# Kernel optimization log

Measured on AMD Instinct MI355X. Metric: run time of the kernel, lower is better.

Reference implementation:

```python
import jax, jax.numpy as jnp
import numpy as np

EPS = 1e-9
N_HEAD = 16


def clamp_c(c):
    return jnp.clip(c, 1e-4, 1.0)


def _heads(x, H):
    B, T, C = x.shape
    return x.reshape(B, T, H, C // H)


def mobius_add(x, y, c_clamped, H):
    # per-head Mobius addition; c_clamped: (H,)
    B, T, C = x.shape
    cr = c_clamped.reshape(1, 1, H, 1)
    xr, yr = _heads(x, H), _heads(y, H)
    xn = jnp.sum(xr * xr, axis=-1, keepdims=True)
    yn = jnp.sum(yr * yr, axis=-1, keepdims=True)
    ip = jnp.sum(xr * yr, axis=-1, keepdims=True)
    num = (1 + 2 * cr * ip + cr * yn) * xr + (1 - cr * xn) * yr
    den = 1 + 2 * cr * ip + cr ** 2 * xn * yn
    return (num / (den + EPS)).reshape(B, T, C)


def expmap(x, v, c, H):
    # exponential map of tangent vector v at point x (per-head curvature)
    B, T, C = x.shape
    cc = clamp_c(c)
    cr = cc.reshape(1, 1, H, 1)
    xr, vr = _heads(x, H), _heads(v, H)
    sf = 2.0 / (1 + cr * jnp.sum(xr * xr, axis=-1, keepdims=True) + EPS)  # scaling factor
    vns = jnp.sum(vr * vr, axis=-1, keepdims=True)
    vn = jnp.sqrt(vns + EPS)
    tanh_arg = jnp.abs(cr * sf * vns / 2)
    coeff = (1.0 / (jnp.sqrt(jnp.abs(cr) + EPS) + EPS)) * jnp.tanh(jnp.sqrt(tanh_arg + EPS))
    second = (coeff * vr / (vn + EPS)).reshape(B, T, C)
    return mobius_add(x, second, cc, H)


def layernorm(x, g):
    m = jnp.mean(x, axis=-1, keepdims=True)
    v = jnp.mean((x - m) ** 2, axis=-1, keepdims=True)
    return (x - m) * jax.lax.rsqrt(v + 1e-5) * g


def attention(x, w_qkv, w_proj, H):
    B, T, C = x.shape
    hs = C // H
    q, k, v = jnp.split(x @ w_qkv.T, 3, axis=-1)
    q = q.reshape(B, T, H, hs).transpose(0, 2, 1, 3)
    k = k.reshape(B, T, H, hs).transpose(0, 2, 1, 3)
    v = v.reshape(B, T, H, hs).transpose(0, 2, 1, 3)
    att = jnp.einsum('bhqd,bhkd->bhqk', q, k) * (float(hs) ** -0.5)
    mask = jnp.tril(jnp.ones((T, T), dtype=bool))
    att = jnp.where(mask, att, -jnp.inf)
    att = jax.nn.softmax(att, axis=-1)
    y = jnp.einsum('bhqk,bhkd->bhqd', att, v)
    y = y.transpose(0, 2, 1, 3).reshape(B, T, C)
    return y @ w_proj.T


def setup_inputs() -> dict:
    key = jax.random.key(0)
    ks = jax.random.split(key, 9)
    B, T, C = 2, 2048, 1024
    s = 0.02
    return {
        'x': jax.random.normal(ks[0], (B, T, C), jnp.float32) * s,
        'ln1_g': jnp.ones((C,), jnp.float32),
        'w_qkv': jax.random.normal(ks[1], (3 * C, C), jnp.float32) * s,
        'w_attn_proj': jax.random.normal(ks[2], (C, C), jnp.float32) * s,
        'c_attn': jax.random.uniform(ks[3], (N_HEAD,), jnp.float32, 0.1, 0.9),
        'ln2_g': jnp.ones((C,), jnp.float32),
        'w_fc': jax.random.normal(ks[4], (4 * C, C), jnp.float32) * s,
        'w_mlp_proj': jax.random.normal(ks[5], (C, 4 * C), jnp.float32) * s,
        'c_mlp': jax.random.uniform(ks[6], (N_HEAD,), jnp.float32, 0.1, 0.9),
    }


def reference(x, ln1_g, w_qkv, w_attn_proj, c_attn, ln2_g, w_fc, w_mlp_proj, c_mlp):
    H = N_HEAD
    a = attention(layernorm(x, ln1_g), w_qkv, w_attn_proj, H)
    x = expmap(x, a, c_attn, H)  # hyperbolic residual (attn)
    h = jax.nn.gelu(layernorm(x, ln2_g) @ w_fc.T, approximate=False) @ w_mlp_proj.T
    x = expmap(x, h, c_mlp, H)   # hyperbolic residual (mlp)
    return x
```

## Files before the change

### kernel.cpp

```cpp
#include <hip/hip_runtime.h>
#include <hip/hip_bf16.h>

typedef __attribute__((ext_vector_type(8))) short bf16x8;
typedef __attribute__((ext_vector_type(4))) float f32x4;

typedef const __attribute__((address_space(1))) void gv_t;
typedef __attribute__((address_space(3))) void lv_t;
#define GLL16(g, l) __builtin_amdgcn_global_load_lds((gv_t*)(g), (lv_t*)(l), 16, 0, 0)

__device__ __forceinline__ short f2bf(float f) {
    __hip_bfloat16 h = __float2bfloat16(f);
    return *reinterpret_cast<short*>(&h);
}

__device__ __forceinline__ float wred(float v) {
    #pragma unroll
    for (int m = 1; m < 64; m <<= 1) v += __shfl_xor(v, m);
    return v;
}

__global__ __launch_bounds__(256) void cvt_kernel(const float* __restrict__ in,
                                                  short* __restrict__ out, int n4) {
    int i = blockIdx.x * 256 + threadIdx.x;
    if (i < n4) {
        float4 v = ((const float4*)in)[i];
        short4 o;
        o.x = f2bf(v.x); o.y = f2bf(v.y); o.z = f2bf(v.z); o.w = f2bf(v.w);
        ((short4*)out)[i] = o;
    }
}

__global__ __launch_bounds__(256) void ln_kernel(const float* __restrict__ x,
                                                 const float* __restrict__ g,
                                                 short* __restrict__ y) {
    const int row = blockIdx.x, tid = threadIdx.x;
    const float4 v = ((const float4*)(x + (size_t)row * 1024))[tid];
    float s = v.x + v.y + v.z + v.w;
    float s2 = v.x * v.x + v.y * v.y + v.z * v.z + v.w * v.w;
    #pragma unroll
    for (int m = 1; m < 64; m <<= 1) { s += __shfl_xor(s, m); s2 += __shfl_xor(s2, m); }
    __shared__ float rs[4], rs2[4];
    if ((tid & 63) == 0) { rs[tid >> 6] = s; rs2[tid >> 6] = s2; }
    __syncthreads();
    s = rs[0] + rs[1] + rs[2] + rs[3];
    s2 = rs2[0] + rs2[1] + rs2[2] + rs2[3];
    const float mean = s * (1.0f / 1024.0f);
    const float var = s2 * (1.0f / 1024.0f) - mean * mean;
    const float r = rsqrtf(var + 1e-5f);
    const float4 gg = ((const float4*)g)[tid];
    short4 o;
    o.x = f2bf((v.x - mean) * r * gg.x);
    o.y = f2bf((v.y - mean) * r * gg.y);
    o.z = f2bf((v.z - mean) * r * gg.z);
    o.w = f2bf((v.w - mean) * r * gg.w);
    ((short4*)y)[(size_t)row * 256 + tid] = o;
}

template <int EPI>
__global__ __launch_bounds__(256, 2) void gemm_bt(const short* __restrict__ A,
                                                  const short* __restrict__ Bw,
                                                  int M, int N, int K,
                                                  void* __restrict__ o0,
                                                  void* __restrict__ o1,
                                                  void* __restrict__ o2) {
    __shared__ __align__(16) short As[2][128 * 64];
    __shared__ __align__(16) short Bs[2][128 * 64];
    const int tid = threadIdx.x;
    const int wid = tid >> 6, lane = tid & 63;
    const int wm = wid >> 1, wn = wid & 1;
    const int col = lane & 15, grp = lane >> 4;
    const int r8 = lane >> 3, s8 = lane & 7;
    const int m0 = blockIdx.x * 128, n0 = blockIdx.y * 128;
    f32x4 acc[4][4] = {};
    const short* ga = A + (size_t)m0 * K;
    const short* gb = Bw + (size_t)n0 * K;

#define GSTAGE(b_, t_) do {                                                     \
        const int k0_ = (t_) * 64;                                              \
        _Pragma("unroll")                                                       \
        for (int c = 0; c < 4; ++c) {                                           \
            const int row = c * 32 + wid * 8 + r8;                              \
            const int slot = s8 ^ (row & 7);                                    \
            GLL16(ga + (size_t)row * K + k0_ + slot * 8,                        \
                  (char*)&As[b_][0] + c * 4096 + wid * 1024);                   \
            GLL16(gb + (size_t)row * K + k0_ + slot * 8,                        \
                  (char*)&Bs[b_][0] + c * 4096 + wid * 1024);                   \
        }                                                                       \
    } while (0)

    const int NT = K >> 6;
    GSTAGE(0, 0);
    __syncthreads();
    int buf = 0;
    for (int t = 0; t < NT; ++t) {
        if (t + 1 < NT) GSTAGE(buf ^ 1, t + 1);
        const char* At = (const char*)&As[buf][0];
        const char* Bt = (const char*)&Bs[buf][0];
        #pragma unroll
        for (int s = 0; s < 2; ++s) {
            bf16x8 af[4], bfr[4];
            #pragma unroll
            for (int i = 0; i < 4; ++i) {
                const int rowA = wm * 64 + i * 16 + col;
                const int rowB = wn * 64 + i * 16 + col;
                af[i]  = *(const bf16x8*)(At + rowA * 128 + (((s * 4 + grp) ^ (rowA & 7)) << 4));
                bfr[i] = *(const bf16x8*)(Bt + rowB * 128 + (((s * 4 + grp) ^ (rowB & 7)) << 4));
            }
            #pragma unroll
            for (int mi = 0; mi < 4; ++mi)
                #pragma unroll
                for (int ni = 0; ni < 4; ++ni)
                    acc[mi][ni] = __builtin_amdgcn_mfma_f32_16x16x32_bf16(af[mi], bfr[ni], acc[mi][ni], 0, 0, 0);
        }
        __syncthreads();
        buf ^= 1;
    }
#undef GSTAGE
    #pragma unroll
    for (int mi = 0; mi < 4; ++mi) {
        #pragma unroll
        for (int ni = 0; ni < 4; ++ni) {
            #pragma unroll
            for (int i = 0; i < 4; ++i) {
                const int m = m0 + wm * 64 + mi * 16 + grp * 4 + i;
                const int n = n0 + wn * 64 + ni * 16 + col;
                const float v = acc[mi][ni][i];
                if (EPI == 0) {
                    const int b = m >> 11, t = m & 2047;
                    const int which = n >> 10, nn = n & 1023;
                    const int h = nn >> 6, d = nn & 63;
                    const size_t bh = (size_t)(b * 16 + h);
                    if (which == 0)
                        ((short*)o0)[(bh * 2048 + t) * 64 + d] = f2bf(v * 0.125f);
                    else if (which == 1)
                        ((short*)o1)[(bh * 2048 + t) * 64 + d] = f2bf(v);
                    else
                        ((short*)o2)[(bh * 64 + d) * 2048 + t] = f2bf(v);
                } else if (EPI == 1) {
                    ((float*)o0)[(size_t)m * N + n] = v;
                } else {
                    const float gl = 0.5f * v * (1.0f + erff(v * 0.70710678118654752f));
                    ((short*)o0)[(size_t)m * N + n] = f2bf(gl);
                }
            }
        }
    }
}

__global__ __launch_bounds__(256, 3) void attn_kernel(const short* __restrict__ Q,
                                                      const short* __restrict__ Kg,
                                                      const short* __restrict__ VT,
                                                      short* __restrict__ Y) {
    __shared__ __align__(16) short Ks[2][4096];
    __shared__ __align__(16) short Vs[2][4096];
    __shared__ __align__(16) short Plds[4][16 * 72];
    const int j = 15 - blockIdx.x;
    const int bh = blockIdx.y;
    const int tid = threadIdx.x, wid = tid >> 6, lane = tid & 63;
    const int ql = lane & 15, g = lane >> 4;
    const int r8 = lane >> 3, s8 = lane & 7;
    const int q0w = j * 128 + wid * 32;
    const int lt = 2 * j + 1;
    const short* Qb = Q + (size_t)bh * 2048 * 64;
    const short* Kb = Kg + (size_t)bh * 2048 * 64;
    const short* Vb = VT + (size_t)bh * 64 * 2048;
    short* Pw = &Plds[wid][0];

    bf16x8 qf[2][2];
    #pragma unroll
    for (int qs = 0; qs < 2; ++qs) {
        qf[qs][0] = *(const bf16x8*)&Qb[(size_t)(q0w + 16 * qs + ql) * 64 + 8 * g];
        qf[qs][1] = *(const bf16x8*)&Qb[(size_t)(q0w + 16 * qs + ql) * 64 + 32 + 8 * g];
    }
    f32x4 o[2][4] = {};
    float m[2] = {-1e30f, -1e30f}, lsum[2] = {0.f, 0.f};

#define STAGE(b_, kt_) do {                                                      \
        const int kbase_ = (kt_) * 64;                                           \
        _Pragma("unroll")                                                        \
        for (int c = 0; c < 2; ++c) {                                            \
            const int row = c * 32 + wid * 8 + r8;                               \
            const int slot = s8 ^ (row & 7);                                     \
            GLL16(Kb + (size_t)(kbase_ + row) * 64 + slot * 8,                   \
                  (char*)&Ks[b_][0] + c * 4096 + wid * 1024);                    \
            GLL16(Vb + (size_t)row * 2048 + kbase_ + slot * 8,                   \
                  (char*)&Vs[b_][0] + c * 4096 + wid * 1024);                    \
        }                                                                        \
    } while (0)

    STAGE(0, 0);
    __syncthreads();
    int buf = 0;
    for (int kt = 0; kt <= lt; ++kt) {
        if (kt < lt) STAGE(buf ^ 1, kt + 1);
        const int kbase = kt * 64;
        const short* Kt = &Ks[buf][0];
        const short* Vt = &Vs[buf][0];
        bf16x8 kf[4][2];
        #pragma unroll
        for (int kb = 0; kb < 4; ++kb) {
            const int row = 16 * kb + ql;
            const int x = row & 7;
            kf[kb][0] = *(const bf16x8*)((const char*)Kt + row * 128 + ((g ^ x) << 4));
            kf[kb][1] = *(const bf16x8*)((const char*)Kt + row * 128 + (((4 + g) ^ x) << 4));
        }
        #pragma unroll
        for (int qs = 0; qs < 2; ++qs) {
            const int q0s = q0w + 16 * qs;
            if (kbase > q0s + 15) continue;
            f32x4 s[4];
            #pragma unroll
            for (int kb = 0; kb < 4; ++kb) {
                f32x4 z = {0.f, 0.f, 0.f, 0.f};
                z = __builtin_amdgcn_mfma_f32_16x16x32_bf16(kf[kb][0], qf[qs][0], z, 0, 0, 0);
                z = __builtin_amdgcn_mfma_f32_16x16x32_bf16(kf[kb][1], qf[qs][1], z, 0, 0, 0);
                s[kb] = z;
            }
            if (kbase + 63 > q0s) {
                #pragma unroll
                for (int kb = 0; kb < 4; ++kb)
                    #pragma unroll
                    for (int r = 0; r < 4; ++r)
                        if (kbase + 16 * kb + 4 * g + r > q0s + ql) s[kb][r] = -1e30f;
            }
            float t0 = fmaxf(fmaxf(s[0][0], s[0][1]), fmaxf(s[0][2], s[0][3]));
            float t1 = fmaxf(fmaxf(s[1][0], s[1][1]), fmaxf(s[1][2], s[1][3]));
            float t2 = fmaxf(fmaxf(s[2][0], s[2][1]), fmaxf(s[2][2], s[2][3]));
            float t3 = fmaxf(fmaxf(s[3][0], s[3][1]), fmaxf(s[3][2], s[3][3]));
            float tmax = fmaxf(fmaxf(t0, t1), fmaxf(t2, t3));
            tmax = fmaxf(tmax, __shfl_xor(tmax, 16));
            tmax = fmaxf(tmax, __shfl_xor(tmax, 32));
            const float mnew = fmaxf(m[qs], tmax);
            const float sc = __expf(m[qs] - mnew);
            m[qs] = mnew;
            float rsum = 0.0f;
            #pragma unroll
            for (int kb = 0; kb < 4; ++kb) {
                const float e0 = __expf(s[kb][0] - mnew);
                const float e1 = __expf(s[kb][1] - mnew);
                const float e2 = __expf(s[kb][2] - mnew);
                const float e3 = __expf(s[kb][3] - mnew);
                rsum += (e0 + e1) + (e2 + e3);
                short4 pk;
                pk.x = f2bf(e0); pk.y = f2bf(e1); pk.z = f2bf(e2); pk.w = f2bf(e3);
                *(short4*)&Pw[ql * 72 + 16 * kb + 4 * g] = pk;
            }
            rsum += __shfl_xor(rsum, 16);
            rsum += __shfl_xor(rsum, 32);
            lsum[qs] = lsum[qs] * sc + rsum;
            #pragma unroll
            for (int nf = 0; nf < 4; ++nf)
                #pragma unroll
                for (int r = 0; r < 4; ++r) o[qs][nf][r] *= sc;
            const bf16x8 pb0 = *(const bf16x8*)&Pw[ql * 72 + 8 * g];
            const bf16x8 pb1 = *(const bf16x8*)&Pw[ql * 72 + 32 + 8 * g];
            #pragma unroll
            for (int nf = 0; nf < 4; ++nf) {
                const int row = 16 * nf + ql;
                const int x = row & 7;
                bf16x8 v0 = *(const bf16x8*)((const char*)Vt + row * 128 + ((g ^ x) << 4));
                bf16x8 v1 = *(const bf16x8*)((const char*)Vt + row * 128 + (((4 + g) ^ x) << 4));
                o[qs][nf] = __builtin_amdgcn_mfma_f32_16x16x32_bf16(v0, pb0, o[qs][nf], 0, 0, 0);
                o[qs][nf] = __builtin_amdgcn_mfma_f32_16x16x32_bf16(v1, pb1, o[qs][nf], 0, 0, 0);
            }
        }
        __syncthreads();
        buf ^= 1;
    }
#undef STAGE
    const int b = bh >> 4, h = bh & 15;
    #pragma unroll
    for (int qs = 0; qs < 2; ++qs) {
        const float inv = 1.0f / lsum[qs];
        const size_t rowoff = ((size_t)b * 2048 + q0w + 16 * qs + ql) * 1024 + h * 64;
        #pragma unroll
        for (int nf = 0; nf < 4; ++nf) {
            short4 w;
            w.x = f2bf(o[qs][nf][0] * inv);
            w.y = f2bf(o[qs][nf][1] * inv);
            w.z = f2bf(o[qs][nf][2] * inv);
            w.w = f2bf(o[qs][nf][3] * inv);
            *(short4*)&Y[rowoff + 16 * nf + 4 * g] = w;
        }
    }
}

__global__ __launch_bounds__(256) void expmap_kernel(const float* __restrict__ x,
                                                     const float* __restrict__ v,
                                                     const float* __restrict__ carr,
                                                     float* __restrict__ out) {
    const int blk = blockIdx.x;
    const int row = blk >> 2;
    const int head = (blk & 3) * 4 + (threadIdx.x >> 6);
    const int lane = threadIdx.x & 63;
    const size_t idx = (size_t)row * 1024 + head * 64 + lane;
    float c = carr[head];
    c = fminf(fmaxf(c, 1e-4f), 1.0f);
    const float xe = x[idx], ve = v[idx];
    const float xn = wred(xe * xe);
    const float vns = wred(ve * ve);
    const float vn = sqrtf(vns + 1e-9f);
    const float sf = 2.0f / (1.0f + c * xn + 1e-9f);
    const float targ = fabsf(0.5f * c * sf * vns);
    const float coeff = (1.0f / (sqrtf(c + 1e-9f) + 1e-9f)) * tanhf(sqrtf(targ + 1e-9f));
    const float ye = coeff * ve / (vn + 1e-9f);
    const float yn = wred(ye * ye);
    const float ip = wred(xe * ye);
    const float num = (1.0f + 2.0f * c * ip + c * yn) * xe + (1.0f - c * xn) * ye;
    const float den = 1.0f + 2.0f * c * ip + c * c * xn * yn;
    out[idx] = num / (den + 1e-9f);
}

extern "C" void kernel_launch(void* const* d_in, const int* in_sizes, int n_in,
                              void* d_out, int out_size, void* d_ws, size_t ws_size,
                              hipStream_t stream) {
    (void)in_sizes; (void)n_in; (void)out_size; (void)ws_size;
    const float* x      = (const float*)d_in[0];
    const float* ln1_g  = (const float*)d_in[1];
    const float* w_qkv  = (const float*)d_in[2];
    const float* w_proj = (const float*)d_in[3];
    const float* c_attn = (const float*)d_in[4];
    const float* ln2_g  = (const float*)d_in[5];
    const float* w_fc   = (const float*)d_in[6];
    const float* w_mlp  = (const float*)d_in[7];
    const float* c_mlp  = (const float*)d_in[8];
    float* out = (float*)d_out;
    char* ws = (char*)d_ws;
    const size_t MB = 1024 * 1024;

    short* wqkv_bf  = (short*)(ws + 0 * MB);
    short* wproj_bf = (short*)(ws + 6 * MB);
    short* wfc_bf   = (short*)(ws + 8 * MB);
    short* wmlp_bf  = (short*)(ws + 16 * MB);
    short* y_bf     = (short*)(ws + 24 * MB);
    short* q_bf     = (short*)(ws + 32 * MB);
    short* k_bf     = (short*)(ws + 40 * MB);
    short* vT_bf    = (short*)(ws + 48 * MB);
    short* att_bf   = (short*)(ws + 56 * MB);
    float* a_f32    = (float*)(ws + 64 * MB);
    float* x1       = (float*)(ws + 80 * MB);
    short* g_bf     = (short*)(ws + 32 * MB);
    float* h_f32    = (float*)(ws + 64 * MB);

    cvt_kernel<<<3072, 256, 0, stream>>>(w_qkv, wqkv_bf, 3072 * 1024 / 4);
    cvt_kernel<<<1024, 256, 0, stream>>>(w_proj, wproj_bf, 1024 * 1024 / 4);
    cvt_kernel<<<4096, 256, 0, stream>>>(w_fc, wfc_bf, 4096 * 1024 / 4);
    cvt_kernel<<<4096, 256, 0, stream>>>(w_mlp, wmlp_bf, 1024 * 4096 / 4);

    ln_kernel<<<4096, 256, 0, stream>>>(x, ln1_g, y_bf);
    gemm_bt<0><<<dim3(32, 24), 256, 0, stream>>>(y_bf, wqkv_bf, 4096, 3072, 1024,
                                                 q_bf, k_bf, vT_bf);
    attn_kernel<<<dim3(16, 32), 256, 0, stream>>>(q_bf, k_bf, vT_bf, att_bf);
    gemm_bt<1><<<dim3(32, 8), 256, 0, stream>>>(att_bf, wproj_bf, 4096, 1024, 1024,
                                                a_f32, nullptr, nullptr);
    expmap_kernel<<<16384, 256, 0, stream>>>(x, a_f32, c_attn, x1);
    ln_kernel<<<4096, 256, 0, stream>>>(x1, ln2_g, y_bf);
    gemm_bt<2><<<dim3(32, 32), 256, 0, stream>>>(y_bf, wfc_bf, 4096, 4096, 1024,
                                                 g_bf, nullptr, nullptr);
    gemm_bt<1><<<dim3(32, 8), 256, 0, stream>>>(g_bf, wmlp_bf, 4096, 1024, 4096,
                                                h_f32, nullptr, nullptr);
    expmap_kernel<<<16384, 256, 0, stream>>>(x1, h_f32, c_mlp, out);
}
```

Baseline: 311.0 us.

## Restructure GEMM main loop into prefetch-two pipeline with explicit waitcnt barriers

The bf16 GEMM loop now preloads two K-tiles before it starts. In each iteration it reads the whole current LDS tile into registers, waits on LDS, and passes a raw barrier. It then issues the global-to-LDS load for tile t+2 into the buffer just freed, runs the MFMAs, and uses vmcnt(8) so it only waits for the older tile. This is meant to hide global load latency behind two tiles of compute instead of one, and to drop the full __syncthreads drains. In exchange the fragments for both k-substeps stay live in registers at once, and correctness now relies on hand-placed waitcnt and barriers.

```diff
diff --git a/kernel.cpp b/kernel.cpp
--- a/kernel.cpp
+++ b/kernel.cpp
@@ -7,6 +7,12 @@
 typedef const __attribute__((address_space(1))) void gv_t;
 typedef __attribute__((address_space(3))) void lv_t;
 #define GLL16(g, l) __builtin_amdgcn_global_load_lds((gv_t*)(g), (lv_t*)(l), 16, 0, 0)
+
+#define WAITV8() asm volatile("s_waitcnt vmcnt(8)" ::: "memory")
+#define WAITV0() asm volatile("s_waitcnt vmcnt(0)" ::: "memory")
+#define WAITL0() asm volatile("s_waitcnt lgkmcnt(0)" ::: "memory")
+#define SCHEDB() __builtin_amdgcn_sched_barrier(0)
+#define BARRAW() __builtin_amdgcn_s_barrier()
 
 __device__ __forceinline__ short f2bf(float f) {
     __hip_bfloat16 h = __float2bfloat16(f);
@@ -90,30 +96,39 @@
 
     const int NT = K >> 6;
     GSTAGE(0, 0);
-    __syncthreads();
-    int buf = 0;
+    if (NT > 1) { GSTAGE(1, 1); WAITV8(); } else { WAITV0(); }
+    SCHEDB();
+    BARRAW();
+    int cur = 0;
     for (int t = 0; t < NT; ++t) {
-        if (t + 1 < NT) GSTAGE(buf ^ 1, t + 1);
-        const char* At = (const char*)&As[buf][0];
-        const char* Bt = (const char*)&Bs[buf][0];
-        #pragma unroll
-        for (int s = 0; s < 2; ++s) {
-            bf16x8 af[4], bfr[4];
+        const char* At = (const char*)&As[cur][0];
+        const char* Bt = (const char*)&Bs[cur][0];
+        bf16x8 af[2][4], bfr[2][4];
+        #pragma unroll
+        for (int s = 0; s < 2; ++s)
             #pragma unroll
             for (int i = 0; i < 4; ++i) {
                 const int rowA = wm * 64 + i * 16 + col;
                 const int rowB = wn * 64 + i * 16 + col;
-                af[i]  = *(const bf16x8*)(At + rowA * 128 + (((s * 4 + grp) ^ (rowA & 7)) << 4));
-                bfr[i] = *(const bf16x8*)(Bt + rowB * 128 + (((s * 4 + grp) ^ (rowB & 7)) << 4));
-            }
+                af[s][i]  = *(const bf16x8*)(At + rowA * 128 + (((s * 4 + grp) ^ (rowA & 7)) << 4));
+                bfr[s][i] = *(const bf16x8*)(Bt + rowB * 128 + (((s * 4 + grp) ^ (rowB & 7)) << 4));
+            }
+        WAITL0(); SCHEDB();
+        BARRAW();
+        if (t + 2 < NT) GSTAGE(cur, t + 2);
+        #pragma unroll
+        for (int s = 0; s < 2; ++s)
             #pragma unroll
             for (int mi = 0; mi < 4; ++mi)
                 #pragma unroll
                 for (int ni = 0; ni < 4; ++ni)
-                    acc[mi][ni] = __builtin_amdgcn_mfma_f32_16x16x32_bf16(af[mi], bfr[ni], acc[mi][ni], 0, 0, 0);
-        }
-        __syncthreads();
-        buf ^= 1;
+                    acc[mi][ni] = __builtin_amdgcn_mfma_f32_16x16x32_bf16(af[s][mi], bfr[s][ni], acc[mi][ni], 0, 0, 0);
+        if (t + 1 < NT) {
+            if (t + 2 < NT) { WAITV8(); } else { WAITV0(); }
+            SCHEDB();
+            BARRAW();
+        }
+        cur ^= 1;
     }
 #undef GSTAGE
     #pragma unroll
```

New measurement: 303.1 us. 1.03x faster.
